# Kernel tuning notes

Hardware: AMD Instinct MI355X
Metric: run time of the kernel (lower is better)

Reference implementation:

```python
import jax, jax.numpy as jnp
import numpy as np

N_USERS = 100_000
N_ITEMS = 150_000
N_REL = 16
N_FACT = 4
D = 64
N_EDGES = 2_000_000
NNZ = 2_000_000
N_LAYERS = 2


def setup_inputs() -> dict:
    key = jax.random.key(0)
    ks = jax.random.split(key, 10)
    return {
        "user_emb": jax.random.normal(ks[0], (N_USERS, D), jnp.float32) * 0.1,
        "entity_emb": jax.random.normal(ks[1], (N_ITEMS, D), jnp.float32) * 0.1,
        "latent_emb": jax.random.normal(ks[2], (N_FACT, D), jnp.float32) * 0.1,
        "weight": jax.random.normal(ks[3], (N_REL, D), jnp.float32) * 0.1,
        "disen_weight_att": jax.random.normal(ks[4], (N_FACT, N_REL), jnp.float32) * 0.1,
        "interact_val": jax.random.uniform(ks[5], (NNZ,), jnp.float32),
        "edge_index": jax.random.randint(ks[6], (2, N_EDGES), 0, N_ITEMS),
        "edge_type": jax.random.randint(ks[7], (N_EDGES,), 1, N_REL + 1),
        "interact_row": jax.random.randint(ks[8], (NNZ,), 0, N_USERS),
        "interact_col": jax.random.randint(ks[9], (NNZ,), 0, N_ITEMS),
    }


def _dist_corr(t1, t2):
    # torch _distance_correlation on 1-D vectors of length n
    n = t1.shape[0]
    t1 = t1[:, None]
    t2 = t2[:, None]
    dx = jnp.sqrt(jnp.maximum(t1 ** 2 - 2.0 * (t1 @ t1.T) + (t1 ** 2).T, 0.0) + 1e-8)
    dy = jnp.sqrt(jnp.maximum(t2 ** 2 - 2.0 * (t2 @ t2.T) + (t2 ** 2).T, 0.0) + 1e-8)
    A = dx - dx.mean(0, keepdims=True) - dx.mean(1, keepdims=True) + dx.mean()
    B = dy - dy.mean(0, keepdims=True) - dy.mean(1, keepdims=True) + dy.mean()
    dcov = lambda P, Q: jnp.sqrt(jnp.maximum((P * Q).sum() / (n * n), 0.0) + 1e-8)
    return dcov(A, B) / jnp.sqrt(dcov(A, A) * dcov(B, B) + 1e-8)


def _l2_normalize(x):
    # F.normalize(x) default: dim=1, eps=1e-12
    nrm = jnp.sqrt(jnp.sum(x * x, axis=1, keepdims=True))
    return x / jnp.maximum(nrm, 1e-12)


def _forward(user_emb, entity_emb, latent_emb, weight, disen_weight_att,
             interact_val, edge_index, edge_type, interact_row, interact_col):
    head, tail = edge_index[0], edge_index[1]
    entity_res, user_res = entity_emb, user_emb

    # correlation score over disentangled factor pairs (n_factors small, fixed loop)
    cor = jnp.asarray(0.0, jnp.float32)
    for i in range(N_FACT):
        for j in range(i + 1, N_FACT):
            cor = cor + _dist_corr(disen_weight_att[i], disen_weight_att[j])

    ones_e = jnp.ones((N_EDGES,), entity_emb.dtype)
    cnt = jax.ops.segment_sum(ones_e, head, num_segments=N_ITEMS)  # [n_items]
    denom = jnp.maximum(cnt, 1.0)[:, None]

    for _ in range(N_LAYERS):
        # KG aggregate: gather + elementwise mul + scatter_mean
        msg = entity_emb[tail] * weight[edge_type - 1]            # [E, D]
        entity_agg = jax.ops.segment_sum(msg, head, num_segments=N_ITEMS) / denom

        # user->factor attention
        score = jax.nn.softmax(user_emb @ latent_emb.T, axis=1)[..., None]  # [U, F, 1]

        # sparse mm: user_agg = interact_mat @ entity_emb
        user_agg = jax.ops.segment_sum(interact_val[:, None] * entity_emb[interact_col],
                                       interact_row, num_segments=N_USERS)  # [U, D]

        dis = jax.nn.softmax(disen_weight_att, axis=-1) @ weight  # [F, D]
        mix = (dis[None, :, :] * score).sum(axis=1)               # [U, D]
        user_agg = user_agg * mix + user_agg

        entity_emb = _l2_normalize(entity_agg)
        user_emb = _l2_normalize(user_agg)
        entity_res = entity_res + entity_emb
        user_res = user_res + user_emb

    return entity_res, user_res, cor


def reference(user_emb, entity_emb, latent_emb, weight, disen_weight_att,
              interact_val, edge_index, edge_type, interact_row, interact_col):
    return _forward(user_emb, entity_emb, latent_emb, weight, disen_weight_att,
                    interact_val, edge_index, edge_type, interact_row, interact_col)
```

## Files before the change

### kernel.cpp

```cpp
#include <hip/hip_runtime.h>

#define N_USERS 100000
#define N_ITEMS 150000
#define N_REL 16
#define N_FACT 4
#define DD 64
#define N_EDGES 2000000
#define NNZ 2000000

#define KE 293
#define KU 196
#define TBE 4096
#define TBU 2048
#define GEB ((N_EDGES + TBE - 1) / TBE)
#define GUB ((NNZ + TBU - 1) / TBU)
#define EBLK (N_ITEMS / 16)
#define UBLK (N_USERS / 16)
#define CAPE 8192
#define CAPU 12288

__device__ __forceinline__ unsigned short f2b(float f) {
    unsigned u = __float_as_uint(f);
    return (unsigned short)((u + 0x7FFFu + ((u >> 16) & 1u)) >> 16);
}
__device__ __forceinline__ float b2f(unsigned short h) {
    return __uint_as_float((unsigned)h << 16);
}
__device__ __forceinline__ float4 b4f(ushort4 r) {
    return make_float4(b2f(r.x), b2f(r.y), b2f(r.z), b2f(r.w));
}

__global__ __launch_bounds__(256) void init_kernel(const float4* __restrict__ uemb,
                                                   const float4* __restrict__ eemb,
                                                   ushort4* __restrict__ entB0,
                                                   float4* __restrict__ cur_usr,
                                                   float4* __restrict__ eres,
                                                   float4* __restrict__ ures,
                                                   int* __restrict__ bktcntE,
                                                   int* __restrict__ bktcntU) {
    int i = blockIdx.x * 256 + threadIdx.x;
    const int NE4 = N_ITEMS * 16;
    const int NU4 = N_USERS * 16;
    if (i < NE4) {
        float4 v = eemb[i];
        eres[i] = v;
        entB0[i] = make_ushort4(f2b(v.x), f2b(v.y), f2b(v.z), f2b(v.w));
    }
    if (i < NU4) { float4 v = uemb[i]; cur_usr[i] = v; ures[i] = v; }
    if (i < KE) bktcntE[i] = 0;
    if (i < KU) bktcntU[i] = 0;
}

__global__ __launch_bounds__(256) void small_kernel(const float* __restrict__ att,
                                                    const float* __restrict__ weight,
                                                    float* __restrict__ cor_out,
                                                    float* __restrict__ dis) {
    __shared__ float sA[256], sB[256];
    __shared__ float srx[16], scx[16], sry[16], scy[16];
    __shared__ float stotx, stoty;
    int t = threadIdx.x;
    if (blockIdx.x == 1) {
        int f = t >> 6, d = t & 63;
        float m = -1e30f;
        for (int r = 0; r < N_REL; ++r) m = fmaxf(m, att[f * N_REL + r]);
        float w[N_REL]; float s = 0.f;
        for (int r = 0; r < N_REL; ++r) { w[r] = expf(att[f * N_REL + r] - m); s += w[r]; }
        float acc = 0.f;
        for (int r = 0; r < N_REL; ++r) acc += (w[r] / s) * weight[r * DD + d];
        dis[f * DD + d] = acc;
        return;
    }
    int a = t >> 4, b = t & 15;
    float cor_acc = 0.f;
    for (int i = 0; i < N_FACT; ++i) {
        for (int j = i + 1; j < N_FACT; ++j) {
            const float* t1 = att + i * N_REL;
            const float* t2 = att + j * N_REL;
            float d1 = t1[a] - t1[b];
            float d2 = t2[a] - t2[b];
            float dx = sqrtf(d1 * d1 + 1e-8f);
            float dy = sqrtf(d2 * d2 + 1e-8f);
            sA[t] = dx; sB[t] = dy;
            __syncthreads();
            if (t < 16)      { float s = 0; for (int k = 0; k < 16; ++k) s += sA[t * 16 + k]; srx[t] = s; }
            else if (t < 32) { int c = t & 15; float s = 0; for (int k = 0; k < 16; ++k) s += sA[k * 16 + c]; scx[c] = s; }
            else if (t < 48) { int r = t & 15; float s = 0; for (int k = 0; k < 16; ++k) s += sB[r * 16 + k]; sry[r] = s; }
            else if (t < 64) { int c = t & 15; float s = 0; for (int k = 0; k < 16; ++k) s += sB[k * 16 + c]; scy[c] = s; }
            __syncthreads();
            if (t == 0)  { float s = 0; for (int k = 0; k < 16; ++k) s += srx[k]; stotx = s; }
            if (t == 64) { float s = 0; for (int k = 0; k < 16; ++k) s += sry[k]; stoty = s; }
            __syncthreads();
            float A = dx - scx[b] * 0.0625f - srx[a] * 0.0625f + stotx * (1.f / 256.f);
            float B = dy - scy[b] * 0.0625f - sry[a] * 0.0625f + stoty * (1.f / 256.f);
            float vab = A * B, vaa = A * A, vbb = B * B;
            for (int off = 32; off; off >>= 1) {
                vab += __shfl_xor(vab, off, 64);
                vaa += __shfl_xor(vaa, off, 64);
                vbb += __shfl_xor(vbb, off, 64);
            }
            __syncthreads();
            if ((t & 63) == 0) {
                int w = t >> 6;
                sA[w] = vab; sA[4 + w] = vaa; sA[8 + w] = vbb;
            }
            __syncthreads();
            if (t == 0) {
                float sAB = sA[0] + sA[1] + sA[2] + sA[3];
                float sAA = sA[4] + sA[5] + sA[6] + sA[7];
                float sBB = sA[8] + sA[9] + sA[10] + sA[11];
                float dab = sqrtf(fmaxf(sAB * (1.f / 256.f), 0.f) + 1e-8f);
                float daa = sqrtf(fmaxf(sAA * (1.f / 256.f), 0.f) + 1e-8f);
                float dbb = sqrtf(fmaxf(sBB * (1.f / 256.f), 0.f) + 1e-8f);
                cor_acc += dab / sqrtf(daa * dbb + 1e-8f);
            }
            __syncthreads();
        }
    }
    if (t == 0) *cor_out = cor_acc;
}

struct BinSME {
    unsigned int stage[TBE];
    unsigned short sbkt[TBE];
    int hist[KE];
    int lofs[KE + 1];
    int gbase[KE];
};
struct BinSMU {
    unsigned long long stage[TBU];
    unsigned short sbkt[TBU];
    int hist[KU];
    int lofs[KU + 1];
    int gbase[KU];
};
__global__ __launch_bounds__(256) void bin_both_kernel(const int* __restrict__ eidx,
                                                       const int* __restrict__ etype,
                                                       const int* __restrict__ irow,
                                                       const int* __restrict__ icol,
                                                       const float* __restrict__ ival,
                                                       int* __restrict__ bktcntE,
                                                       int* __restrict__ bktcntU,
                                                       unsigned int* __restrict__ binE,
                                                       unsigned long long* __restrict__ binU) {
    __shared__ union { BinSME e; BinSMU u; } sm;
    int tid = threadIdx.x;
    if (blockIdx.x < GEB) {
        int e0 = blockIdx.x * TBE;
        int nloc = min(TBE, N_EDGES - e0);
        for (int b = tid; b < KE; b += 256) sm.e.hist[b] = 0;
        __syncthreads();
        for (int i = tid; i < nloc; i += 256)
            atomicAdd(&sm.e.hist[__builtin_nontemporal_load(&eidx[e0 + i]) >> 9], 1);
        __syncthreads();
        if (tid < 64) {
            const int chunk = (KE + 63) >> 6;
            int base = tid * chunk;
            int s = 0;
            for (int c = 0; c < chunk; ++c) { int ix = base + c; if (ix < KE) s += sm.e.hist[ix]; }
            int inc = s;
            for (int d = 1; d < 64; d <<= 1) { int tv = __shfl_up(inc, d, 64); if (tid >= d) inc += tv; }
            int run = inc - s;
            for (int c = 0; c < chunk; ++c) { int ix = base + c; if (ix < KE) { sm.e.lofs[ix] = run; run += sm.e.hist[ix]; } }
            if (tid == 63) sm.e.lofs[KE] = run;
        }
        __syncthreads();
        for (int b = tid; b < KE; b += 256) {
            int cnt = sm.e.lofs[b + 1] - sm.e.lofs[b];
            if (cnt > 0) sm.e.gbase[b] = atomicAdd(&bktcntE[b], cnt);
            sm.e.hist[b] = sm.e.lofs[b];
        }
        __syncthreads();
        for (int i = tid; i < nloc; i += 256) {
            int h = __builtin_nontemporal_load(&eidx[e0 + i]);
            int tt = __builtin_nontemporal_load(&eidx[N_EDGES + e0 + i]);
            int r  = __builtin_nontemporal_load(&etype[e0 + i]) - 1;
            int b = h >> 9;
            int slot = atomicAdd(&sm.e.hist[b], 1);
            sm.e.stage[slot] = (unsigned int)tt | ((unsigned int)r << 18) | ((unsigned int)(h & 511) << 22);
            sm.e.sbkt[slot] = (unsigned short)b;
        }
        __syncthreads();
        int total = sm.e.lofs[KE];
        for (int i = tid; i < total; i += 256) {
            int b = sm.e.sbkt[i];
            int slot = sm.e.gbase[b] + (i - sm.e.lofs[b]);
            if (slot < CAPE) binE[(size_t)b * CAPE + slot] = sm.e.stage[i];
        }
    } else {
        int e0 = (blockIdx.x - GEB) * TBU;
        int nloc = min(TBU, NNZ - e0);
        for (int b = tid; b < KU; b += 256) sm.u.hist[b] = 0;
        __syncthreads();
        for (int i = tid; i < nloc; i += 256)
            atomicAdd(&sm.u.hist[__builtin_nontemporal_load(&irow[e0 + i]) >> 9], 1);
        __syncthreads();
        if (tid < 64) {
            const int chunk = (KU + 63) >> 6;
            int base = tid * chunk;
            int s = 0;
            for (int c = 0; c < chunk; ++c) { int ix = base + c; if (ix < KU) s += sm.u.hist[ix]; }
            int inc = s;
            for (int d = 1; d < 64; d <<= 1) { int tv = __shfl_up(inc, d, 64); if (tid >= d) inc += tv; }
            int run = inc - s;
            for (int c = 0; c < chunk; ++c) { int ix = base + c; if (ix < KU) { sm.u.lofs[ix] = run; run += sm.u.hist[ix]; } }
            if (tid == 63) sm.u.lofs[KU] = run;
        }
        __syncthreads();
        for (int b = tid; b < KU; b += 256) {
            int cnt = sm.u.lofs[b + 1] - sm.u.lofs[b];
            if (cnt > 0) sm.u.gbase[b] = atomicAdd(&bktcntU[b], cnt);
            sm.u.hist[b] = sm.u.lofs[b];
        }
        __syncthreads();
        for (int i = tid; i < nloc; i += 256) {
            int row = __builtin_nontemporal_load(&irow[e0 + i]);
            int col = __builtin_nontemporal_load(&icol[e0 + i]);
            float v  = __builtin_nontemporal_load(&ival[e0 + i]);
            int b = row >> 9;
            int slot = atomicAdd(&sm.u.hist[b], 1);
            sm.u.stage[slot] = ((unsigned long long)__float_as_uint(v) << 32)
                             | ((unsigned long long)(row & 511) << 18)
                             | (unsigned int)col;
            sm.u.sbkt[slot] = (unsigned short)b;
        }
        __syncthreads();
        int total = sm.u.lofs[KU];
        for (int i = tid; i < total; i += 256) {
            int b = sm.u.sbkt[i];
            int slot = sm.u.gbase[b] + (i - sm.u.lofs[b]);
            if (slot < CAPU) binU[(size_t)b * CAPU + slot] = sm.u.stage[i];
        }
    }
}

__global__ __launch_bounds__(512) void bucket_scan_kernel(const int* __restrict__ bktcntE,
                                                          const int* __restrict__ bktcntU,
                                                          int* __restrict__ bbaseE,
                                                          int* __restrict__ bbaseU,
                                                          int* __restrict__ eoff,
                                                          int* __restrict__ uoff) {
    __shared__ int lds[512];
    int t = threadIdx.x;
    const int* cnt; int* bbase; int K; int* off; int n; int cap;
    if (blockIdx.x == 0) { cnt = bktcntE; bbase = bbaseE; K = KE; off = eoff; n = N_ITEMS; cap = CAPE; }
    else                 { cnt = bktcntU; bbase = bbaseU; K = KU; off = uoff; n = N_USERS; cap = CAPU; }
    int v = (t < K) ? min(cnt[t], cap) : 0;
    lds[t] = v; __syncthreads();
    for (int o = 1; o < 512; o <<= 1) {
        int add = (t >= o) ? lds[t - o] : 0;
        __syncthreads();
        lds[t] += add;
        __syncthreads();
    }
    if (t < K) bbase[t] = lds[t] - v;
    if (t == K - 1) off[n] = lds[t];
}

__global__ __launch_bounds__(256) void fine_both_kernel(const int* __restrict__ bktcntE,
                                                        const int* __restrict__ bktcntU,
                                                        const int* __restrict__ bbaseE,
                                                        const int* __restrict__ bbaseU,
                                                        const unsigned int* __restrict__ binE,
                                                        const unsigned long long* __restrict__ binU,
                                                        int* __restrict__ eoff,
                                                        int* __restrict__ uoff,
                                                        int* __restrict__ pack,
                                                        unsigned long long* __restrict__ upair) {
    __shared__ int hist[512];
    __shared__ int scanb[256];
    __shared__ int curs[512];
    int tid = threadIdx.x;
    if (blockIdx.x < KE) {
        int b = blockIdx.x;
        int row0 = b << 9;
        int cnt = min(bktcntE[b], CAPE);
        int base = bbaseE[b];
        for (int r = tid; r < 512; r += 256) hist[r] = 0;
        __syncthreads();
        for (int i = tid; i < cnt; i += 256)
            atomicAdd(&hist[binE[(size_t)b * CAPE + i] >> 22], 1);
        __syncthreads();
        int a0 = hist[2 * tid], a1 = hist[2 * tid + 1];
        int s = a0 + a1;
        scanb[tid] = s; __syncthreads();
        for (int o = 1; o < 256; o <<= 1) {
            int add = (tid >= o) ? scanb[tid - o] : 0;
            __syncthreads();
            scanb[tid] += add;
            __syncthreads();
        }
        int excl = scanb[tid] - s;
        curs[2 * tid]     = base + excl;
        curs[2 * tid + 1] = base + excl + a0;
        int row = row0 + 2 * tid;
        if (row < N_ITEMS)     eoff[row]     = base + excl;
        if (row + 1 < N_ITEMS) eoff[row + 1] = base + excl + a0;
        __syncthreads();
        for (int i = tid; i < cnt; i += 256) {
            unsigned int p = binE[(size_t)b * CAPE + i];
            int pos = atomicAdd(&curs[p >> 22], 1);
            pack[pos] = (int)(p & 0x3FFFFF);
        }
    } else {
        int b = blockIdx.x - KE;
        int row0 = b << 9;
        int cnt = min(bktcntU[b], CAPU);
        int base = bbaseU[b];
        for (int r = tid; r < 512; r += 256) hist[r] = 0;
        __syncthreads();
        for (int i = tid; i < cnt; i += 256)
            atomicAdd(&hist[(int)(binU[(size_t)b * CAPU + i] >> 18) & 511], 1);
        __syncthreads();
        int a0 = hist[2 * tid], a1 = hist[2 * tid + 1];
        int s = a0 + a1;
        scanb[tid] = s; __syncthreads();
        for (int o = 1; o < 256; o <<= 1) {
            int add = (tid >= o) ? scanb[tid - o] : 0;
            __syncthreads();
            scanb[tid] += add;
            __syncthreads();
        }
        int excl = scanb[tid] - s;
        curs[2 * tid]     = base + excl;
        curs[2 * tid + 1] = base + excl + a0;
        int row = row0 + 2 * tid;
        if (row < N_USERS)     uoff[row]     = base + excl;
        if (row + 1 < N_USERS) uoff[row + 1] = base + excl + a0;
        __syncthreads();
        for (int i = tid; i < cnt; i += 256) {
            unsigned long long p = binU[(size_t)b * CAPU + i];
            int pos = atomicAdd(&curs[(int)(p >> 18) & 511], 1);
            upair[pos] = p & 0xFFFFFFFF0003FFFFull;
        }
    }
}

__global__ __launch_bounds__(256) void layer_kernel(const int* __restrict__ eoff,
                                                    const int* __restrict__ pack,
                                                    const int* __restrict__ uoff,
                                                    const unsigned long long* __restrict__ upair,
                                                    const ushort4* __restrict__ entBIn,
                                                    const float4* __restrict__ w4,
                                                    const float4* __restrict__ lat4,
                                                    const float4* __restrict__ dis4,
                                                    ushort4* __restrict__ entBOut,
                                                    float4* __restrict__ eres4,
                                                    float4* __restrict__ usr4,
                                                    float4* __restrict__ ures4) {
    int w = threadIdx.x >> 6;
    int lane = threadIdx.x & 63;
    int g = lane >> 4, li = lane & 15;
    if (blockIdx.x < EBLK) {
        int row = blockIdx.x * 16 + w * 4 + g;
        int beg = eoff[row];
        int deg = eoff[row + 1] - beg;
        int mdeg = max(deg, __shfl_xor(deg, 16, 64));
        mdeg = max(mdeg, __shfl_xor(mdeg, 32, 64));
        float4 acc = make_float4(0.f, 0.f, 0.f, 0.f);
        for (int cb = 0; cb < mdeg; cb += 16) {
            int pk = 0;
            if (cb + li < deg) pk = __builtin_nontemporal_load(&pack[beg + cb + li]);
            int pv[16];
            #pragma unroll
            for (int k = 0; k < 16; ++k) pv[k] = __shfl(pk, k, 16);
            ushort4 rows[16];
            #pragma unroll
            for (int k = 0; k < 16; ++k)
                rows[k] = entBIn[(size_t)(pv[k] & 0x3FFFF) * 16 + li];
            #pragma unroll
            for (int k = 0; k < 16; ++k) {
                if (cb + k < deg) {
                    float4 e  = b4f(rows[k]);
                    float4 ww = w4[(pv[k] >> 18) * 16 + li];
                    acc.x += e.x * ww.x; acc.y += e.y * ww.y;
                    acc.z += e.z * ww.z; acc.w += e.w * ww.w;
                }
            }
        }
        float inv = 1.f / fmaxf((float)deg, 1.f);
        acc.x *= inv; acc.y *= inv; acc.z *= inv; acc.w *= inv;
        float ss = acc.x * acc.x + acc.y * acc.y + acc.z * acc.z + acc.w * acc.w;
        for (int o = 8; o; o >>= 1) ss += __shfl_xor(ss, o, 16);
        float rn = 1.f / fmaxf(sqrtf(ss), 1e-12f);
        float4 v = make_float4(acc.x * rn, acc.y * rn, acc.z * rn, acc.w * rn);
        entBOut[(size_t)row * 16 + li] = make_ushort4(f2b(v.x), f2b(v.y), f2b(v.z), f2b(v.w));
        float4 rr = eres4[(size_t)row * 16 + li];
        rr.x += v.x; rr.y += v.y; rr.z += v.z; rr.w += v.w;
        eres4[(size_t)row * 16 + li] = rr;
    } else {
        int u = (blockIdx.x - EBLK) * 16 + w * 4 + g;
        float4 uv = usr4[(size_t)u * 16 + li];
        float4 l0 = lat4[0 * 16 + li], l1 = lat4[1 * 16 + li];
        float4 l2 = lat4[2 * 16 + li], l3 = lat4[3 * 16 + li];
        float p0 = uv.x * l0.x + uv.y * l0.y + uv.z * l0.z + uv.w * l0.w;
        float p1 = uv.x * l1.x + uv.y * l1.y + uv.z * l1.z + uv.w * l1.w;
        float p2 = uv.x * l2.x + uv.y * l2.y + uv.z * l2.z + uv.w * l2.w;
        float p3 = uv.x * l3.x + uv.y * l3.y + uv.z * l3.z + uv.w * l3.w;
        for (int o = 8; o; o >>= 1) {
            p0 += __shfl_xor(p0, o, 16);
            p1 += __shfl_xor(p1, o, 16);
            p2 += __shfl_xor(p2, o, 16);
            p3 += __shfl_xor(p3, o, 16);
        }
        float m = fmaxf(fmaxf(p0, p1), fmaxf(p2, p3));
        float e0 = expf(p0 - m), e1 = expf(p1 - m), e2 = expf(p2 - m), e3 = expf(p3 - m);
        float sinv = 1.f / (e0 + e1 + e2 + e3);
        float s0 = e0 * sinv, s1 = e1 * sinv, s2 = e2 * sinv, s3 = e3 * sinv;
        float4 d0 = dis4[0 * 16 + li], d1 = dis4[1 * 16 + li];
        float4 d2 = dis4[2 * 16 + li], d3 = dis4[3 * 16 + li];
        float4 mix = make_float4(d0.x * s0 + d1.x * s1 + d2.x * s2 + d3.x * s3,
                                 d0.y * s0 + d1.y * s1 + d2.y * s2 + d3.y * s3,
                                 d0.z * s0 + d1.z * s1 + d2.z * s2 + d3.z * s3,
                                 d0.w * s0 + d1.w * s1 + d2.w * s2 + d3.w * s3);
        int beg = uoff[u];
        int deg = uoff[u + 1] - beg;
        int mdeg = max(deg, __shfl_xor(deg, 16, 64));
        mdeg = max(mdeg, __shfl_xor(mdeg, 32, 64));
        float4 acc = make_float4(0.f, 0.f, 0.f, 0.f);
        for (int cb = 0; cb < mdeg; cb += 16) {
            unsigned long long pr = 0;
            if (cb + li < deg) pr = __builtin_nontemporal_load(&upair[beg + cb + li]);
            int clo[16]; float cval[16];
            #pragma unroll
            for (int k = 0; k < 16; ++k) {
                clo[k]  = __shfl((int)(pr & 0xFFFFFFFFu), k, 16);
                cval[k] = __uint_as_float((unsigned)__shfl((int)(pr >> 32), k, 16));
            }
            ushort4 rows[16];
            #pragma unroll
            for (int k = 0; k < 16; ++k)
                rows[k] = entBIn[(size_t)clo[k] * 16 + li];
            #pragma unroll
            for (int k = 0; k < 16; ++k) {
                float4 e = b4f(rows[k]);
                acc.x += cval[k] * e.x; acc.y += cval[k] * e.y;
                acc.z += cval[k] * e.z; acc.w += cval[k] * e.w;
            }
        }
        float4 v = make_float4(acc.x * mix.x + acc.x, acc.y * mix.y + acc.y,
                               acc.z * mix.z + acc.z, acc.w * mix.w + acc.w);
        float ss = v.x * v.x + v.y * v.y + v.z * v.z + v.w * v.w;
        for (int o = 8; o; o >>= 1) ss += __shfl_xor(ss, o, 16);
        float rn = 1.f / fmaxf(sqrtf(ss), 1e-12f);
        v.x *= rn; v.y *= rn; v.z *= rn; v.w *= rn;
        usr4[(size_t)u * 16 + li] = v;
        float4 rr = ures4[(size_t)u * 16 + li];
        rr.x += v.x; rr.y += v.y; rr.z += v.z; rr.w += v.w;
        ures4[(size_t)u * 16 + li] = rr;
    }
}

extern "C" void kernel_launch(void* const* d_in, const int* in_sizes, int n_in,
                              void* d_out, int out_size, void* d_ws, size_t ws_size,
                              hipStream_t stream) {
    const float* user_emb   = (const float*)d_in[0];
    const float* entity_emb = (const float*)d_in[1];
    const float* latent     = (const float*)d_in[2];
    const float* weight     = (const float*)d_in[3];
    const float* att        = (const float*)d_in[4];
    const float* ival       = (const float*)d_in[5];
    const int*   eidx       = (const int*)d_in[6];
    const int*   etype      = (const int*)d_in[7];
    const int*   irow       = (const int*)d_in[8];
    const int*   icol       = (const int*)d_in[9];

    float* out        = (float*)d_out;
    float* entity_res = out;
    float* user_res   = out + (size_t)N_ITEMS * DD;
    float* cor_out    = out + (size_t)N_ITEMS * DD + (size_t)N_USERS * DD;

    char* ws = (char*)d_ws;
    ushort4* entB0 = (ushort4*)ws;  ws += (size_t)N_ITEMS * DD * 2;
    ushort4* entB1 = (ushort4*)ws;  ws += (size_t)N_ITEMS * DD * 2;
    float* cur_usr = (float*)ws;    ws += (size_t)N_USERS * DD * 4;
    int*   eoff    = (int*)ws;      ws += (size_t)(N_ITEMS + 1) * 4;
    int*   epack   = (int*)ws;      ws += (size_t)N_EDGES * 4;
    int*   uoff    = (int*)ws;      ws += (size_t)(N_USERS + 1) * 4;
    unsigned long long* upair = (unsigned long long*)ws; ws += (size_t)NNZ * 8;
    unsigned long long* binU  = (unsigned long long*)ws; ws += (size_t)KU * CAPU * 8;
    int*   bktcntE = (int*)ws;      ws += 512 * 4;
    int*   bktcntU = (int*)ws;      ws += 512 * 4;
    int*   bbaseE  = (int*)ws;      ws += 512 * 4;
    int*   bbaseU  = (int*)ws;      ws += 512 * 4;
    float* dis     = (float*)ws;    ws += 256 * 4;
    unsigned int* binE = (unsigned int*)entB1;

    init_kernel<<<(N_ITEMS * 16 + 255) / 256, 256, 0, stream>>>(
        (const float4*)user_emb, (const float4*)entity_emb,
        entB0, (float4*)cur_usr, (float4*)entity_res, (float4*)user_res,
        bktcntE, bktcntU);

    small_kernel<<<2, 256, 0, stream>>>(att, weight, cor_out, dis);

    bin_both_kernel<<<GEB + GUB, 256, 0, stream>>>(eidx, etype, irow, icol, ival,
                                                   bktcntE, bktcntU, binE, binU);
    bucket_scan_kernel<<<2, 512, 0, stream>>>(bktcntE, bktcntU, bbaseE, bbaseU, eoff, uoff);
    fine_both_kernel<<<KE + KU, 256, 0, stream>>>(bktcntE, bktcntU, bbaseE, bbaseU,
                                                  binE, binU, eoff, uoff, epack, upair);

    ushort4* entbuf[2] = { entB0, entB1 };
    for (int layer = 0; layer < 2; ++layer) {
        ushort4* eIn  = entbuf[layer & 1];
        ushort4* eOut = entbuf[(layer & 1) ^ 1];
        layer_kernel<<<EBLK + UBLK, 256, 0, stream>>>(eoff, epack, uoff, upair,
                                                      (const ushort4*)eIn,
                                                      (const float4*)weight,
                                                      (const float4*)latent,
                                                      (const float4*)dis,
                                                      eOut,
                                                      (float4*)entity_res,
                                                      (float4*)cur_usr,
                                                      (float4*)user_res);
    }
}
```

Measured before the change: 412.8 us.

## Use 16-byte bf16 row gathers with 8 lanes per row and interleaved layout

The bf16 entity table is stored interleaved so each lane holds dims f and f+8 packed as 8 contiguous bf16 values. The gather kernels then assign 8 lanes per row instead of 16 and load 16 bytes per lane rather than 8, so each block covers 32 rows and each gathered row takes half as many memory instructions. Edges and nonzeros are now consumed in chunks of 8, which adds more loop iterations and shuffles per row. Low-degree rows may also waste fewer masked lanes. Bounds guards are added because the item count is not a multiple of 32.

```diff
diff --git a/kernel.cpp b/kernel.cpp
--- a/kernel.cpp
+++ b/kernel.cpp
@@ -14,10 +14,13 @@
 #define TBU 2048
 #define GEB ((N_EDGES + TBE - 1) / TBE)
 #define GUB ((NNZ + TBU - 1) / TBU)
-#define EBLK (N_ITEMS / 16)
-#define UBLK (N_USERS / 16)
+#define EBLK2 ((N_ITEMS + 31) / 32)
+#define UBLK2 (N_USERS / 32)
 #define CAPE 8192
 #define CAPU 12288
+
+typedef float          __attribute__((ext_vector_type(4))) f32x4;
+typedef unsigned short __attribute__((ext_vector_type(8))) u16x8;
 
 __device__ __forceinline__ unsigned short f2b(float f) {
     unsigned u = __float_as_uint(f);
@@ -26,13 +29,11 @@
 __device__ __forceinline__ float b2f(unsigned short h) {
     return __uint_as_float((unsigned)h << 16);
 }
-__device__ __forceinline__ float4 b4f(ushort4 r) {
-    return make_float4(b2f(r.x), b2f(r.y), b2f(r.z), b2f(r.w));
-}
+
 
 __global__ __launch_bounds__(256) void init_kernel(const float4* __restrict__ uemb,
                                                    const float4* __restrict__ eemb,
-                                                   ushort4* __restrict__ entB0,
+                                                   ushort4* __restrict__ entB0_u4,
                                                    float4* __restrict__ cur_usr,
                                                    float4* __restrict__ eres,
                                                    float4* __restrict__ ures,
@@ -44,7 +45,9 @@
     if (i < NE4) {
         float4 v = eemb[i];
         eres[i] = v;
-        entB0[i] = make_ushort4(f2b(v.x), f2b(v.y), f2b(v.z), f2b(v.w));
+        int rr = i >> 4, f = i & 15;
+        entB0_u4[(size_t)rr * 16 + ((f & 7) << 1) + (f >> 3)] =
+            make_ushort4(f2b(v.x), f2b(v.y), f2b(v.z), f2b(v.w));
     }
     if (i < NU4) { float4 v = uemb[i]; cur_usr[i] = v; ures[i] = v; }
     if (i < KE) bktcntE[i] = 0;
@@ -339,114 +342,166 @@
                                                     const int* __restrict__ pack,
                                                     const int* __restrict__ uoff,
                                                     const unsigned long long* __restrict__ upair,
-                                                    const ushort4* __restrict__ entBIn,
+                                                    const u16x8* __restrict__ entBIn,
                                                     const float4* __restrict__ w4,
                                                     const float4* __restrict__ lat4,
                                                     const float4* __restrict__ dis4,
-                                                    ushort4* __restrict__ entBOut,
+                                                    u16x8* __restrict__ entBOut,
                                                     float4* __restrict__ eres4,
                                                     float4* __restrict__ usr4,
                                                     float4* __restrict__ ures4) {
     int w = threadIdx.x >> 6;
     int lane = threadIdx.x & 63;
-    int g = lane >> 4, li = lane & 15;
-    if (blockIdx.x < EBLK) {
-        int row = blockIdx.x * 16 + w * 4 + g;
-        int beg = eoff[row];
-        int deg = eoff[row + 1] - beg;
-        int mdeg = max(deg, __shfl_xor(deg, 16, 64));
-        mdeg = max(mdeg, __shfl_xor(mdeg, 32, 64));
-        float4 acc = make_float4(0.f, 0.f, 0.f, 0.f);
-        for (int cb = 0; cb < mdeg; cb += 16) {
+    int g = lane >> 3, li = lane & 7;
+    if (blockIdx.x < EBLK2) {
+        int row = blockIdx.x * 32 + w * 8 + g;
+        bool valid = row < N_ITEMS;
+        int beg = 0, deg = 0;
+        if (valid) { beg = eoff[row]; deg = eoff[row + 1] - beg; }
+        int mdeg = deg;
+        for (int o = 8; o < 64; o <<= 1) mdeg = max(mdeg, __shfl_xor(mdeg, o, 64));
+        float4 a0 = make_float4(0.f, 0.f, 0.f, 0.f);
+        float4 a1 = make_float4(0.f, 0.f, 0.f, 0.f);
+        for (int cb = 0; cb < mdeg; cb += 8) {
             int pk = 0;
             if (cb + li < deg) pk = __builtin_nontemporal_load(&pack[beg + cb + li]);
-            int pv[16];
+            int pv[8];
             #pragma unroll
-            for (int k = 0; k < 16; ++k) pv[k] = __shfl(pk, k, 16);
-            ushort4 rows[16];
+            for (int k = 0; k < 8; ++k) pv[k] = __shfl(pk, k, 8);
+            u16x8 rows[8];
             #pragma unroll
-            for (int k = 0; k < 16; ++k)
-                rows[k] = entBIn[(size_t)(pv[k] & 0x3FFFF) * 16 + li];
+            for (int k = 0; k < 8; ++k)
+                rows[k] = entBIn[(size_t)(pv[k] & 0x3FFFF) * 8 + li];
             #pragma unroll
-            for (int k = 0; k < 16; ++k) {
+            for (int k = 0; k < 8; ++k) {
                 if (cb + k < deg) {
-                    float4 e  = b4f(rows[k]);
-                    float4 ww = w4[(pv[k] >> 18) * 16 + li];
-                    acc.x += e.x * ww.x; acc.y += e.y * ww.y;
-                    acc.z += e.z * ww.z; acc.w += e.w * ww.w;
+                    int r = pv[k] >> 18;
+                    float4 wa = w4[r * 16 + li];
+                    float4 wb = w4[r * 16 + 8 + li];
+                    a0.x += b2f(rows[k][0]) * wa.x; a0.y += b2f(rows[k][1]) * wa.y;
+                    a0.z += b2f(rows[k][2]) * wa.z; a0.w += b2f(rows[k][3]) * wa.w;
+                    a1.x += b2f(rows[k][4]) * wb.x; a1.y += b2f(rows[k][5]) * wb.y;
+                    a1.z += b2f(rows[k][6]) * wb.z; a1.w += b2f(rows[k][7]) * wb.w;
                 }
             }
         }
-        float inv = 1.f / fmaxf((float)deg, 1.f);
-        acc.x *= inv; acc.y *= inv; acc.z *= inv; acc.w *= inv;
-        float ss = acc.x * acc.x + acc.y * acc.y + acc.z * acc.z + acc.w * acc.w;
-        for (int o = 8; o; o >>= 1) ss += __shfl_xor(ss, o, 16);
-        float rn = 1.f / fmaxf(sqrtf(ss), 1e-12f);
-        float4 v = make_float4(acc.x * rn, acc.y * rn, acc.z * rn, acc.w * rn);
-        entBOut[(size_t)row * 16 + li] = make_ushort4(f2b(v.x), f2b(v.y), f2b(v.z), f2b(v.w));
-        float4 rr = eres4[(size_t)row * 16 + li];
-        rr.x += v.x; rr.y += v.y; rr.z += v.z; rr.w += v.w;
-        eres4[(size_t)row * 16 + li] = rr;
+        if (valid) {
+            float inv = 1.f / fmaxf((float)deg, 1.f);
+            a0.x *= inv; a0.y *= inv; a0.z *= inv; a0.w *= inv;
+            a1.x *= inv; a1.y *= inv; a1.z *= inv; a1.w *= inv;
+            float ss = a0.x * a0.x + a0.y * a0.y + a0.z * a0.z + a0.w * a0.w
+                     + a1.x * a1.x + a1.y * a1.y + a1.z * a1.z + a1.w * a1.w;
+            for (int o = 4; o; o >>= 1) ss += __shfl_xor(ss, o, 8);
+            float rn = 1.f / fmaxf(sqrtf(ss), 1e-12f);
+            a0.x *= rn; a0.y *= rn; a0.z *= rn; a0.w *= rn;
+            a1.x *= rn; a1.y *= rn; a1.z *= rn; a1.w *= rn;
+            u16x8 ob;
+            ob[0] = f2b(a0.x); ob[1] = f2b(a0.y); ob[2] = f2b(a0.z); ob[3] = f2b(a0.w);
+            ob[4] = f2b(a1.x); ob[5] = f2b(a1.y); ob[6] = f2b(a1.z); ob[7] = f2b(a1.w);
+            entBOut[(size_t)row * 8 + li] = ob;
+            float4 r0 = eres4[(size_t)row * 16 + li];
+            float4 r1 = eres4[(size_t)row * 16 + 8 + li];
+            r0.x += a0.x; r0.y += a0.y; r0.z += a0.z; r0.w += a0.w;
+            r1.x += a1.x; r1.y += a1.y; r1.z += a1.z; r1.w += a1.w;
+            eres4[(size_t)row * 16 + li]     = r0;
+            eres4[(size_t)row * 16 + 8 + li] = r1;
+        }
     } else {
-        int u = (blockIdx.x - EBLK) * 16 + w * 4 + g;
-        float4 uv = usr4[(size_t)u * 16 + li];
-        float4 l0 = lat4[0 * 16 + li], l1 = lat4[1 * 16 + li];
-        float4 l2 = lat4[2 * 16 + li], l3 = lat4[3 * 16 + li];
-        float p0 = uv.x * l0.x + uv.y * l0.y + uv.z * l0.z + uv.w * l0.w;
-        float p1 = uv.x * l1.x + uv.y * l1.y + uv.z * l1.z + uv.w * l1.w;
-        float p2 = uv.x * l2.x + uv.y * l2.y + uv.z * l2.z + uv.w * l2.w;
-        float p3 = uv.x * l3.x + uv.y * l3.y + uv.z * l3.z + uv.w * l3.w;
-        for (int o = 8; o; o >>= 1) {
-            p0 += __shfl_xor(p0, o, 16);
-            p1 += __shfl_xor(p1, o, 16);
-            p2 += __shfl_xor(p2, o, 16);
-            p3 += __shfl_xor(p3, o, 16);
+        int u = (blockIdx.x - EBLK2) * 32 + w * 8 + g;
+        float4 uv0 = usr4[(size_t)u * 16 + li];
+        float4 uv1 = usr4[(size_t)u * 16 + 8 + li];
+        float p0, p1, p2, p3;
+        {
+            float4 la = lat4[0 * 16 + li], lb = lat4[0 * 16 + 8 + li];
+            p0 = uv0.x * la.x + uv0.y * la.y + uv0.z * la.z + uv0.w * la.w
+               + uv1.x * lb.x + uv1.y * lb.y + uv1.z * lb.z + uv1.w * lb.w;
+        }
+        {
+            float4 la = lat4[1 * 16 + li], lb = lat4[1 * 16 + 8 + li];
+            p1 = uv0.x * la.x + uv0.y * la.y + uv0.z * la.z + uv0.w * la.w
+               + uv1.x * lb.x + uv1.y * lb.y + uv1.z * lb.z + uv1.w * lb.w;
+        }
+        {
+            float4 la = lat4[2 * 16 + li], lb = lat4[2 * 16 + 8 + li];
+            p2 = uv0.x * la.x + uv0.y * la.y + uv0.z * la.z + uv0.w * la.w
+               + uv1.x * lb.x + uv1.y * lb.y + uv1.z * lb.z + uv1.w * lb.w;
+        }
+        {
+            float4 la = lat4[3 * 16 + li], lb = lat4[3 * 16 + 8 + li];
+            p3 = uv0.x * la.x + uv0.y * la.y + uv0.z * la.z + uv0.w * la.w
+               + uv1.x * lb.x + uv1.y * lb.y + uv1.z * lb.z + uv1.w * lb.w;
+        }
+        for (int o = 4; o; o >>= 1) {
+            p0 += __shfl_xor(p0, o, 8);
+            p1 += __shfl_xor(p1, o, 8);
+            p2 += __shfl_xor(p2, o, 8);
+            p3 += __shfl_xor(p3, o, 8);
         }
         float m = fmaxf(fmaxf(p0, p1), fmaxf(p2, p3));
         float e0 = expf(p0 - m), e1 = expf(p1 - m), e2 = expf(p2 - m), e3 = expf(p3 - m);
         float sinv = 1.f / (e0 + e1 + e2 + e3);
         float s0 = e0 * sinv, s1 = e1 * sinv, s2 = e2 * sinv, s3 = e3 * sinv;
-        float4 d0 = dis4[0 * 16 + li], d1 = dis4[1 * 16 + li];
-        float4 d2 = dis4[2 * 16 + li], d3 = dis4[3 * 16 + li];
-        float4 mix = make_float4(d0.x * s0 + d1.x * s1 + d2.x * s2 + d3.x * s3,
-                                 d0.y * s0 + d1.y * s1 + d2.y * s2 + d3.y * s3,
-                                 d0.z * s0 + d1.z * s1 + d2.z * s2 + d3.z * s3,
-                                 d0.w * s0 + d1.w * s1 + d2.w * s2 + d3.w * s3);
+        float4 mix0, mix1;
+        {
+            float4 d0a = dis4[0 * 16 + li], d1a = dis4[1 * 16 + li];
+            float4 d2a = dis4[2 * 16 + li], d3a = dis4[3 * 16 + li];
+            mix0 = make_float4(d0a.x * s0 + d1a.x * s1 + d2a.x * s2 + d3a.x * s3,
+                               d0a.y * s0 + d1a.y * s1 + d2a.y * s2 + d3a.y * s3,
+                               d0a.z * s0 + d1a.z * s1 + d2a.z * s2 + d3a.z * s3,
+                               d0a.w * s0 + d1a.w * s1 + d2a.w * s2 + d3a.w * s3);
+            float4 d0b = dis4[0 * 16 + 8 + li], d1b = dis4[1 * 16 + 8 + li];
+            float4 d2b = dis4[2 * 16 + 8 + li], d3b = dis4[3 * 16 + 8 + li];
+            mix1 = make_float4(d0b.x * s0 + d1b.x * s1 + d2b.x * s2 + d3b.x * s3,
+                               d0b.y * s0 + d1b.y * s1 + d2b.y * s2 + d3b.y * s3,
+                               d0b.z * s0 + d1b.z * s1 + d2b.z * s2 + d3b.z * s3,
+                               d0b.w * s0 + d1b.w * s1 + d2b.w * s2 + d3b.w * s3);
+        }
         int beg = uoff[u];
         int deg = uoff[u + 1] - beg;
-        int mdeg = max(deg, __shfl_xor(deg, 16, 64));
-        mdeg = max(mdeg, __shfl_xor(mdeg, 32, 64));
-        float4 acc = make_float4(0.f, 0.f, 0.f, 0.f);
-        for (int cb = 0; cb < mdeg; cb += 16) {
+        int mdeg = deg;
+        for (int o = 8; o < 64; o <<= 1) mdeg = max(mdeg, __shfl_xor(mdeg, o, 64));
+        float4 a0 = make_float4(0.f, 0.f, 0.f, 0.f);
+        float4 a1 = make_float4(0.f, 0.f, 0.f, 0.f);
+        for (int cb = 0; cb < mdeg; cb += 8) {
             unsigned long long pr = 0;
             if (cb + li < deg) pr = __builtin_nontemporal_load(&upair[beg + cb + li]);
-            int clo[16]; float cval[16];
+            int clo[8]; float cval[8];
             #pragma unroll
-            for (int k = 0; k < 16; ++k) {
-                clo[k]  = __shfl((int)(pr & 0xFFFFFFFFu), k, 16);
-                cval[k] = __uint_as_float((unsigned)__shfl((int)(pr >> 32), k, 16));
+            for (int k = 0; k < 8; ++k) {
+                clo[k]  = __shfl((int)(pr & 0xFFFFFFFFu), k, 8);
+                cval[k] = __uint_as_float((unsigned)__shfl((int)(pr >> 32), k, 8));
             }
-            ushort4 rows[16];
+            u16x8 rows[8];
             #pragma unroll
-            for (int k = 0; k < 16; ++k)
-                rows[k] = entBIn[(size_t)clo[k] * 16 + li];
+            for (int k = 0; k < 8; ++k)
+                rows[k] = entBIn[(size_t)clo[k] * 8 + li];
             #pragma unroll
-            for (int k = 0; k < 16; ++k) {
-                float4 e = b4f(rows[k]);
-                acc.x += cval[k] * e.x; acc.y += cval[k] * e.y;
-                acc.z += cval[k] * e.z; acc.w += cval[k] * e.w;
+            for (int k = 0; k < 8; ++k) {
+                float cv = cval[k];
+                a0.x += cv * b2f(rows[k][0]); a0.y += cv * b2f(rows[k][1]);
+                a0.z += cv * b2f(rows[k][2]); a0.w += cv * b2f(rows[k][3]);
+                a1.x += cv * b2f(rows[k][4]); a1.y += cv * b2f(rows[k][5]);
+                a1.z += cv * b2f(rows[k][6]); a1.w += cv * b2f(rows[k][7]);
             }
         }
-        float4 v = make_float4(acc.x * mix.x + acc.x, acc.y * mix.y + acc.y,
-                               acc.z * mix.z + acc.z, acc.w * mix.w + acc.w);
-        float ss = v.x * v.x + v.y * v.y + v.z * v.z + v.w * v.w;
-        for (int o = 8; o; o >>= 1) ss += __shfl_xor(ss, o, 16);
+        float4 v0 = make_float4(a0.x * mix0.x + a0.x, a0.y * mix0.y + a0.y,
+                                a0.z * mix0.z + a0.z, a0.w * mix0.w + a0.w);
+        float4 v1 = make_float4(a1.x * mix1.x + a1.x, a1.y * mix1.y + a1.y,
+                                a1.z * mix1.z + a1.z, a1.w * mix1.w + a1.w);
+        float ss = v0.x * v0.x + v0.y * v0.y + v0.z * v0.z + v0.w * v0.w
+                 + v1.x * v1.x + v1.y * v1.y + v1.z * v1.z + v1.w * v1.w;
+        for (int o = 4; o; o >>= 1) ss += __shfl_xor(ss, o, 8);
         float rn = 1.f / fmaxf(sqrtf(ss), 1e-12f);
-        v.x *= rn; v.y *= rn; v.z *= rn; v.w *= rn;
-        usr4[(size_t)u * 16 + li] = v;
-        float4 rr = ures4[(size_t)u * 16 + li];
-        rr.x += v.x; rr.y += v.y; rr.z += v.z; rr.w += v.w;
-        ures4[(size_t)u * 16 + li] = rr;
+        v0.x *= rn; v0.y *= rn; v0.z *= rn; v0.w *= rn;
+        v1.x *= rn; v1.y *= rn; v1.z *= rn; v1.w *= rn;
+        usr4[(size_t)u * 16 + li]     = v0;
+        usr4[(size_t)u * 16 + 8 + li] = v1;
+        float4 r0 = ures4[(size_t)u * 16 + li];
+        float4 r1 = ures4[(size_t)u * 16 + 8 + li];
+        r0.x += v0.x; r0.y += v0.y; r0.z += v0.z; r0.w += v0.w;
+        r1.x += v1.x; r1.y += v1.y; r1.z += v1.z; r1.w += v1.w;
+        ures4[(size_t)u * 16 + li]     = r0;
+        ures4[(size_t)u * 16 + 8 + li] = r1;
     }
 }
 
@@ -470,8 +525,8 @@
     float* cor_out    = out + (size_t)N_ITEMS * DD + (size_t)N_USERS * DD;
 
     char* ws = (char*)d_ws;
-    ushort4* entB0 = (ushort4*)ws;  ws += (size_t)N_ITEMS * DD * 2;
-    ushort4* entB1 = (ushort4*)ws;  ws += (size_t)N_ITEMS * DD * 2;
+    char* entB0 = ws;               ws += (size_t)N_ITEMS * DD * 2;
+    char* entB1 = ws;               ws += (size_t)N_ITEMS * DD * 2;
     float* cur_usr = (float*)ws;    ws += (size_t)N_USERS * DD * 4;
     int*   eoff    = (int*)ws;      ws += (size_t)(N_ITEMS + 1) * 4;
     int*   epack   = (int*)ws;      ws += (size_t)N_EDGES * 4;
@@ -487,7 +542,7 @@
 
     init_kernel<<<(N_ITEMS * 16 + 255) / 256, 256, 0, stream>>>(
         (const float4*)user_emb, (const float4*)entity_emb,
-        entB0, (float4*)cur_usr, (float4*)entity_res, (float4*)user_res,
+        (ushort4*)entB0, (float4*)cur_usr, (float4*)entity_res, (float4*)user_res,
         bktcntE, bktcntU);
 
     small_kernel<<<2, 256, 0, stream>>>(att, weight, cor_out, dis);
@@ -498,18 +553,18 @@
     fine_both_kernel<<<KE + KU, 256, 0, stream>>>(bktcntE, bktcntU, bbaseE, bbaseU,
                                                   binE, binU, eoff, uoff, epack, upair);
 
-    ushort4* entbuf[2] = { entB0, entB1 };
+    char* entbuf[2] = { entB0, entB1 };
     for (int layer = 0; layer < 2; ++layer) {
-        ushort4* eIn  = entbuf[layer & 1];
-        ushort4* eOut = entbuf[(layer & 1) ^ 1];
-        layer_kernel<<<EBLK + UBLK, 256, 0, stream>>>(eoff, epack, uoff, upair,
-                                                      (const ushort4*)eIn,
-                                                      (const float4*)weight,
-                                                      (const float4*)latent,
-                                                      (const float4*)dis,
-                                                      eOut,
-                                                      (float4*)entity_res,
-                                                      (float4*)cur_usr,
-                                                      (float4*)user_res);
-    }
-}
+        char* eIn  = entbuf[layer & 1];
+        char* eOut = entbuf[(layer & 1) ^ 1];
+        layer_kernel<<<EBLK2 + UBLK2, 256, 0, stream>>>(eoff, epack, uoff, upair,
+                                                        (const u16x8*)eIn,
+                                                        (const float4*)weight,
+                                                        (const float4*)latent,
+                                                        (const float4*)dis,
+                                                        (u16x8*)eOut,
+                                                        (float4*)entity_res,
+                                                        (float4*)cur_usr,
+                                                        (float4*)user_res);
+    }
+}
```

Result: faster. 371.5 us (-10.0%).
